# Optimization experiments

Measured on AMD Instinct MI355X. Metric: run time of the kernel, lower is better.

The kernel has to match this reference:

```python
import jax, jax.numpy as jnp
import numpy as np

N = 16777216
C = 2
BINS = 10
MOMENTUM = 0.75


def setup_inputs() -> dict:
    key = jax.random.key(0)
    k1, k2 = jax.random.split(key)
    outputs = jax.random.normal(k1, (N, C), dtype=jnp.float32)
    targets = jax.random.randint(k2, (N,), 0, C, dtype=jnp.int64)
    acc_sum = jnp.zeros((BINS,), dtype=jnp.float32)
    return {"outputs": outputs, "targets": targets, "acc_sum": acc_sum}


def reference(outputs, targets, acc_sum):
    n, c = outputs.shape
    tgt = targets.astype(jnp.int32)
    logp = jax.nn.log_softmax(outputs, axis=1)            # [N, C]
    p_t = jnp.take_along_axis(jnp.exp(logp), tgt[:, None], axis=1)[:, 0]
    # |softmax - onehot| summed over classes == 2 * (1 - p_target)
    g = 2.0 * (1.0 - p_t)                                 # [N], in [0, 2]
    # torch loop covers edges linspace(0,1,bins+1): only g in [0, 1) gets a weight
    bin_idx = jnp.clip(jnp.floor(g * BINS).astype(jnp.int32), 0, BINS - 1)
    valid = g < 1.0
    counts = jax.ops.segment_sum(jnp.where(valid, 1.0, 0.0).astype(jnp.float32),
                                 bin_idx, num_segments=BINS)  # [BINS]
    # acc_sum updated only for non-empty bins (EMA with momentum)
    new_acc = jnp.where(counts > 0, MOMENTUM * acc_sum + (1.0 - MOMENTUM) * counts, acc_sum)
    per_sample_acc = new_acc[bin_idx]
    weights = jnp.where(valid & (counts[bin_idx] > 0),
                        jnp.float32(n) / per_sample_acc,
                        jnp.float32(0.0))                 # [N]
    # cross_entropy(reduction='none') = -log_softmax[target]
    loss = -jnp.take_along_axis(logp, tgt[:, None], axis=1)[:, 0]
    return jnp.mean(loss * weights)
```

## Files before the change

kernel.cpp:

```cpp
#include <hip/hip_runtime.h>

#define BINS   10
#define CSHIFT 26
#define QMASK  0x03FFFFFFu
#define QSCALE 2097152.0f
#define QLN2   1453635.25f
#define GRID   1536
#define TPB    256
#define TILE   1024


__global__ void ghm_zero_ws(unsigned* ws) {
    if (threadIdx.x < 32) ws[threadIdx.x] = 0u;
}

__device__ __forceinline__ void gld_lds16(const void* g, void* l) {
    __builtin_amdgcn_global_load_lds(
        (const __attribute__((address_space(1))) void*)g,
        (__attribute__((address_space(3))) void*)l, 16, 0, 0);
}

__device__ __forceinline__ void proc1(float o0, float o1, int t, unsigned* A) {
    const float Th[BINS] = {
        2.9444390f, 2.1972246f, 1.7346011f, 1.3862944f, 1.0986123f,
        0.8472979f, 0.6190392f, 0.4054651f, 0.2006707f, 0.0f };
    float s = o0 - o1;
    float d = __int_as_float(__float_as_int(s) ^ (t << 31));
    float em = __expf(-d);
    float qf = fmaf(__log2f(1.0f + em), QLN2, 0.5f);
    unsigned val = (unsigned)qf + (1u << CSHIFT);
    #pragma unroll
    for (int b = 0; b < BINS; ++b)
        A[b] += (d > Th[b]) ? val : 0u;
}

__global__ __launch_bounds__(TPB, 6)
void ghm_main(const float* __restrict__ outs,
              const int*   __restrict__ tgt,
              float*       __restrict__ ws_q,
              unsigned*    __restrict__ ws_c,
              int n) {
    __shared__ union {
        struct {
            unsigned char o[2][TILE * 8];
            unsigned char t[2][TILE * 4];
        } st;
        struct {
            unsigned h[BINS][256];
            unsigned c[BINS][16];
            float    q[BINS][16];
        } ep;
    } sh;

    const int tid  = threadIdx.x;
    const int lane = tid & 63;
    const int wv   = tid >> 6;

    unsigned A[BINS];
    #pragma unroll
    for (int b = 0; b < BINS; ++b) A[b] = 0u;

    const int ntiles = n >> 10;

    const char* outs_b = (const char*)outs;
    const char* tgt_b  = (const char*)tgt;
    #define STAGE(tile, pb)                                                     \
        do {                                                                    \
            const char* go = outs_b + ((size_t)(tile) << 13) + (wv << 11)       \
                             + (lane << 4);                                     \
            char*       lo = (char*)sh.st.o[pb] + (wv << 11);                   \
            gld_lds16(go, lo);                                                  \
            gld_lds16(go + 1024, lo + 1024);                                    \
            const char* gt = tgt_b + ((size_t)(tile) << 12) + (wv << 10)        \
                             + (lane << 4);                                     \
            gld_lds16(gt, (char*)sh.st.t[pb] + (wv << 10));                     \
        } while (0)

    int t  = blockIdx.x;
    int pb = 0;
    if (t < ntiles) STAGE(t, 0);
    __syncthreads();

    for (; t < ntiles; t += gridDim.x) {
        int tn = t + gridDim.x;
        if (tn < ntiles) STAGE(tn, pb ^ 1);

        const float4* o4 = (const float4*)sh.st.o[pb];
        const int4*   t4 = (const int4*)sh.st.t[pb];
        float4 a  = o4[2 * tid];
        float4 bq = o4[2 * tid + 1];
        int4   tv = t4[tid];
        proc1(a.x,  a.y,  tv.x, A);
        proc1(a.z,  a.w,  tv.y, A);
        proc1(bq.x, bq.y, tv.z, A);
        proc1(bq.z, bq.w, tv.w, A);

        __syncthreads();
        pb ^= 1;
    }

    int rem = ntiles << 10;
    if (blockIdx.x == 0) {
        for (int s = rem + tid; s < n; s += TPB)
            proc1(outs[2 * s], outs[2 * s + 1], tgt[s], A);
    }

    __syncthreads();
    #pragma unroll
    for (int b = 0; b < BINS; ++b) sh.ep.h[b][tid] = A[b];
    __syncthreads();

    if (tid < 16 * BINS) {
        int bin  = tid >> 4;
        int part = tid & 15;
        unsigned c = 0, q = 0;
        #pragma unroll
        for (int j = 0; j < 16; ++j) {
            unsigned v = sh.ep.h[bin][j * 16 + part];
            c += v >> CSHIFT;
            q += v & QMASK;
        }
        sh.ep.c[bin][part] = c;
        sh.ep.q[bin][part] = (float)q;
    }
    __syncthreads();
    if (tid < BINS) {
        unsigned c = 0; float q = 0.0f;
        #pragma unroll
        for (int j = 0; j < 16; ++j) { c += sh.ep.c[tid][j]; q += sh.ep.q[tid][j]; }
        if (c) {
            atomicAdd(&ws_c[tid], c);
            atomicAdd(&ws_q[tid], q * (1.0f / QSCALE));
        }
    }
}

__global__ void ghm_final(const float*    __restrict__ ws_q,
                          const unsigned* __restrict__ ws_c,
                          const float*    __restrict__ acc_sum,
                          float* __restrict__ out) {
    if (threadIdx.x == 0) {
        float r = 0.0f, pq = 0.0f;
        unsigned pc = 0u;
        #pragma unroll
        for (int b = 0; b < BINS; ++b) {
            float    cq = ws_q[b];
            unsigned cc = ws_c[b];
            unsigned cnt = cc - pc;
            float    qs  = cq - pq;
            pc = cc; pq = cq;
            if (cnt > 0u) {
                float na = 0.75f * acc_sum[b] + 0.25f * (float)cnt;
                r += qs / na;
            }
        }
        *out = r;
    }
}

extern "C" void kernel_launch(void* const* d_in, const int* in_sizes, int n_in,
                              void* d_out, int out_size, void* d_ws, size_t ws_size,
                              hipStream_t stream) {
    const float* outputs = (const float*)d_in[0];
    const int*   targets = (const int*)d_in[1];
    const float* acc_sum = (const float*)d_in[2];
    int n = in_sizes[1];

    float*    ws_q = (float*)d_ws;
    unsigned* ws_c = (unsigned*)((char*)d_ws + 64);

    ghm_zero_ws<<<1, 64, 0, stream>>>((unsigned*)d_ws);
    ghm_main<<<GRID, TPB, 0, stream>>>(outputs, targets, ws_q, ws_c, n);
    ghm_final<<<1, 64, 0, stream>>>(ws_q, ws_c, acc_sum, (float*)d_out);
}
```

Baseline: 241.6 us.

## Replace LDS double-buffered staging with direct vector global loads and pad atomics

Drops the global_load_lds double-buffered tile pipeline and its per-tile barriers, replacing it with a plain grid-stride loop that loads float4/int4 straight into registers. The grid grows and the occupancy hint rises to 8 blocks per CU, relying on more waves in flight to hide memory latency instead of explicit prefetch. The per-bin global atomics are spread onto separate 128-byte lines to avoid contention between bins. In exchange it loses the explicit overlap of the next tile's load with compute, and the higher occupancy target may force register spills.

Result: slower. 250.3 us (+3.6%).

```diff
diff --git a/kernel.cpp b/kernel.cpp
--- a/kernel.cpp
+++ b/kernel.cpp
@@ -5,19 +5,12 @@
 #define QMASK  0x03FFFFFFu
 #define QSCALE 2097152.0f
 #define QLN2   1453635.25f
-#define GRID   1536
+#define GRID   2048
 #define TPB    256
-#define TILE   1024
 
 
 __global__ void ghm_zero_ws(unsigned* ws) {
-    if (threadIdx.x < 32) ws[threadIdx.x] = 0u;
-}
-
-__device__ __forceinline__ void gld_lds16(const void* g, void* l) {
-    __builtin_amdgcn_global_load_lds(
-        (const __attribute__((address_space(1))) void*)g,
-        (__attribute__((address_space(3))) void*)l, 16, 0, 0);
+    if (threadIdx.x < 320) ws[threadIdx.x] = 0u;
 }
 
 __device__ __forceinline__ void proc1(float o0, float o1, int t, unsigned* A) {
@@ -34,80 +27,42 @@
         A[b] += (d > Th[b]) ? val : 0u;
 }
 
-__global__ __launch_bounds__(TPB, 6)
+__global__ __launch_bounds__(TPB, 8)
 void ghm_main(const float* __restrict__ outs,
               const int*   __restrict__ tgt,
-              float*       __restrict__ ws_q,
-              unsigned*    __restrict__ ws_c,
+              unsigned char* __restrict__ ws,
               int n) {
-    __shared__ union {
-        struct {
-            unsigned char o[2][TILE * 8];
-            unsigned char t[2][TILE * 4];
-        } st;
-        struct {
-            unsigned h[BINS][256];
-            unsigned c[BINS][16];
-            float    q[BINS][16];
-        } ep;
-    } sh;
+    __shared__ unsigned h[BINS][TPB];
+    __shared__ unsigned sc[BINS][16];
+    __shared__ float    sq[BINS][16];
 
-    const int tid  = threadIdx.x;
-    const int lane = tid & 63;
-    const int wv   = tid >> 6;
+    const int tid = threadIdx.x;
 
     unsigned A[BINS];
     #pragma unroll
     for (int b = 0; b < BINS; ++b) A[b] = 0u;
 
-    const int ntiles = n >> 10;
-
-    const char* outs_b = (const char*)outs;
-    const char* tgt_b  = (const char*)tgt;
-    #define STAGE(tile, pb)                                                     \
-        do {                                                                    \
-            const char* go = outs_b + ((size_t)(tile) << 13) + (wv << 11)       \
-                             + (lane << 4);                                     \
-            char*       lo = (char*)sh.st.o[pb] + (wv << 11);                   \
-            gld_lds16(go, lo);                                                  \
-            gld_lds16(go + 1024, lo + 1024);                                    \
-            const char* gt = tgt_b + ((size_t)(tile) << 12) + (wv << 10)        \
-                             + (lane << 4);                                     \
-            gld_lds16(gt, (char*)sh.st.t[pb] + (wv << 10));                     \
-        } while (0)
-
-    int t  = blockIdx.x;
-    int pb = 0;
-    if (t < ntiles) STAGE(t, 0);
-    __syncthreads();
-
-    for (; t < ntiles; t += gridDim.x) {
-        int tn = t + gridDim.x;
-        if (tn < ntiles) STAGE(tn, pb ^ 1);
-
-        const float4* o4 = (const float4*)sh.st.o[pb];
-        const int4*   t4 = (const int4*)sh.st.t[pb];
-        float4 a  = o4[2 * tid];
-        float4 bq = o4[2 * tid + 1];
-        int4   tv = t4[tid];
+    const int nq = n >> 2;
+    const int stride = gridDim.x * TPB;
+    const float4* __restrict__ o4 = (const float4*)outs;
+    const int4*   __restrict__ t4 = (const int4*)tgt;
+    for (int i = blockIdx.x * TPB + tid; i < nq; i += stride) {
+        float4 a  = o4[2 * i];
+        float4 bq = o4[2 * i + 1];
+        int4   tv = t4[i];
         proc1(a.x,  a.y,  tv.x, A);
         proc1(a.z,  a.w,  tv.y, A);
         proc1(bq.x, bq.y, tv.z, A);
         proc1(bq.z, bq.w, tv.w, A);
-
-        __syncthreads();
-        pb ^= 1;
     }
 
-    int rem = ntiles << 10;
     if (blockIdx.x == 0) {
-        for (int s = rem + tid; s < n; s += TPB)
+        for (int s = (nq << 2) + tid; s < n; s += TPB)
             proc1(outs[2 * s], outs[2 * s + 1], tgt[s], A);
     }
 
-    __syncthreads();
     #pragma unroll
-    for (int b = 0; b < BINS; ++b) sh.ep.h[b][tid] = A[b];
+    for (int b = 0; b < BINS; ++b) h[b][tid] = A[b];
     __syncthreads();
 
     if (tid < 16 * BINS) {
@@ -116,36 +71,35 @@
         unsigned c = 0, q = 0;
         #pragma unroll
         for (int j = 0; j < 16; ++j) {
-            unsigned v = sh.ep.h[bin][j * 16 + part];
+            unsigned v = h[bin][j * 16 + part];
             c += v >> CSHIFT;
             q += v & QMASK;
         }
-        sh.ep.c[bin][part] = c;
-        sh.ep.q[bin][part] = (float)q;
+        sc[bin][part] = c;
+        sq[bin][part] = (float)q;
     }
     __syncthreads();
     if (tid < BINS) {
         unsigned c = 0; float q = 0.0f;
         #pragma unroll
-        for (int j = 0; j < 16; ++j) { c += sh.ep.c[tid][j]; q += sh.ep.q[tid][j]; }
+        for (int j = 0; j < 16; ++j) { c += sc[tid][j]; q += sq[tid][j]; }
         if (c) {
-            atomicAdd(&ws_c[tid], c);
-            atomicAdd(&ws_q[tid], q * (1.0f / QSCALE));
+            atomicAdd((unsigned*)(ws + 128 * tid + 64), c);
+            atomicAdd((float*)   (ws + 128 * tid),      q * (1.0f / QSCALE));
         }
     }
 }
 
-__global__ void ghm_final(const float*    __restrict__ ws_q,
-                          const unsigned* __restrict__ ws_c,
-                          const float*    __restrict__ acc_sum,
+__global__ void ghm_final(const unsigned char* __restrict__ ws,
+                          const float* __restrict__ acc_sum,
                           float* __restrict__ out) {
     if (threadIdx.x == 0) {
         float r = 0.0f, pq = 0.0f;
         unsigned pc = 0u;
         #pragma unroll
         for (int b = 0; b < BINS; ++b) {
-            float    cq = ws_q[b];
-            unsigned cc = ws_c[b];
+            float    cq = *(const float*)   (ws + 128 * b);
+            unsigned cc = *(const unsigned*)(ws + 128 * b + 64);
             unsigned cnt = cc - pc;
             float    qs  = cq - pq;
             pc = cc; pq = cq;
@@ -166,10 +120,9 @@
     const float* acc_sum = (const float*)d_in[2];
     int n = in_sizes[1];
 
-    float*    ws_q = (float*)d_ws;
-    unsigned* ws_c = (unsigned*)((char*)d_ws + 64);
-
-    ghm_zero_ws<<<1, 64, 0, stream>>>((unsigned*)d_ws);
-    ghm_main<<<GRID, TPB, 0, stream>>>(outputs, targets, ws_q, ws_c, n);
-    ghm_final<<<1, 64, 0, stream>>>(ws_q, ws_c, acc_sum, (float*)d_out);
+    ghm_zero_ws<<<1, 320, 0, stream>>>((unsigned*)d_ws);
+    ghm_main<<<GRID, TPB, 0, stream>>>(outputs, targets,
+                                       (unsigned char*)d_ws, n);
+    ghm_final<<<1, 64, 0, stream>>>((const unsigned char*)d_ws, acc_sum,
+                                    (float*)d_out);
 }
```
